# Kernel optimization log

Hardware: AMD Instinct MI355X
Metric: run time of the kernel (lower is better)

## Reference

```python
import jax, jax.numpy as jnp
import numpy as np

B, D, E = 65536, 1024, 16
H1, H2 = 128, 64          # expert hidden dims (hidden_dim=128, hidden_dim//2)
R1, R2 = 64, 32           # router hidden dims
EPS = 1e-5                # BatchNorm eps


def setup_inputs() -> dict:
    key = jax.random.key(0)
    ks = jax.random.split(key, 16)
    s = 0.02
    inp = {
        "x": jax.random.normal(ks[0], (B, D), jnp.float32),
        # router BatchNorm1d (eval mode: running stats)
        "r_gamma": jnp.ones((D,), jnp.float32),
        "r_beta": jnp.zeros((D,), jnp.float32),
        "r_mean": jnp.zeros((D,), jnp.float32),
        "r_var": jnp.ones((D,), jnp.float32),
        # router MLP D->64->32->16
        "rW1": jax.random.normal(ks[1], (D, R1), jnp.float32) * s,
        "rb1": jnp.full((R1,), 0.1, jnp.float32),
        "rW2": jax.random.normal(ks[2], (R1, R2), jnp.float32) * s,
        "rb2": jnp.full((R2,), 0.1, jnp.float32),
        "rW3": jax.random.normal(ks[3], (R2, E), jnp.float32) * s,
        "rb3": jnp.full((E,), 0.1, jnp.float32),
        # per-expert BatchNorm1d (eval mode)
        "e_gamma": jnp.ones((E, D), jnp.float32),
        "e_beta": jnp.zeros((E, D), jnp.float32),
        "e_mean": jnp.zeros((E, D), jnp.float32),
        "e_var": jnp.ones((E, D), jnp.float32),
        # per-expert MLP D->128->64->1, stacked along expert dim
        "eW1": jax.random.normal(ks[4], (E, D, H1), jnp.float32) * s,
        "eb1": jnp.full((E, H1), 0.1, jnp.float32),
        "eW2": jax.random.normal(ks[5], (E, H1, H2), jnp.float32) * s,
        "eb2": jnp.full((E, H2), 0.1, jnp.float32),
        "eW3": jax.random.normal(ks[6], (E, H2, 1), jnp.float32) * s,
        "eb3": jnp.full((E, 1), 0.1, jnp.float32),
    }
    return inp


def reference(x, r_gamma, r_beta, r_mean, r_var, rW1, rb1, rW2, rb2, rW3, rb3,
              e_gamma, e_beta, e_mean, e_var, eW1, eb1, eW2, eb2, eW3, eb3):
    # ---- router: BN (eval) -> Linear/ReLU -> Linear/ReLU -> Linear -> softmax
    xn = (x - r_mean) * (r_gamma / jnp.sqrt(r_var + EPS)) + r_beta   # [B,D]
    h = jax.nn.relu(xn @ rW1 + rb1)
    h = jax.nn.relu(h @ rW2 + rb2)
    routing_weights = jax.nn.softmax(h @ rW3 + rb3, axis=1)          # [B,E]

    # ---- experts: fold per-expert BN into first linear to avoid [E,B,D] copy
    scale = e_gamma / jnp.sqrt(e_var + EPS)                          # [E,D]
    shift = e_beta - e_mean * scale                                  # [E,D]
    W1_eff = eW1 * scale[:, :, None]                                 # [E,D,H1]
    b1_eff = eb1 + jnp.einsum('ed,edh->eh', shift, eW1)              # [E,H1]

    h1 = jax.nn.relu(jnp.einsum('bd,edh->ebh', x, W1_eff) + b1_eff[:, None, :])  # [E,B,H1]
    h2 = jax.nn.relu(jnp.einsum('ebh,ehk->ebk', h1, eW2) + eb2[:, None, :])      # [E,B,H2]
    logits = jnp.einsum('ebk,eko->ebo', h2, eW3) + eb3[:, None, :]               # [E,B,1]
    expert_outputs = jax.nn.sigmoid(logits[:, :, 0]).T               # [B,E]

    weighted_pred = jnp.sum(routing_weights * expert_outputs, axis=1)  # [B]
    return weighted_pred, routing_weights, expert_outputs
```

## Files before the change

kernel.cpp:

```cpp
#include <hip/hip_runtime.h>


typedef unsigned short u16;
typedef __attribute__((ext_vector_type(8))) short bf16x8;
typedef __attribute__((ext_vector_type(4))) float f32x4;
typedef __attribute__((ext_vector_type(8))) unsigned short u16x8;
typedef __attribute__((ext_vector_type(4))) unsigned short u16x4;

#define MFMA16(a, b, c) __builtin_amdgcn_mfma_f32_16x16x32_bf16(a, b, c, 0, 0, 0)

#define B_ROWS 65536
#define DIM 1024
#define NE 16
#define EPS 1e-5f

__device__ inline u16 f2bf(float f) {
    union { float f; unsigned u; } c; c.f = f;
    unsigned u = c.u;
    return (u16)((u + 0x7fffu + ((u >> 16) & 1u)) >> 16);
}

__device__ inline void gload16(const u16* g, u16* s) {
    __builtin_amdgcn_global_load_lds(
        (const __attribute__((address_space(1))) unsigned int*)g,
        (__attribute__((address_space(3))) unsigned int*)s,
        16, 0, 0);
}


__device__ void body_prep_x(int blk, int tid, const float* __restrict__ x,
                            u16* __restrict__ xs_g, u16* __restrict__ lds) {
    int p = tid & 15, rloc = tid >> 4;
    int r_g = blk * 16 + rloc;
    int r = r_g & 127;
    int lb = p & 7;
    int phys = lb ^ (r & 7);
    const float* xrow = x + (size_t)r_g * 1024;
#pragma unroll
    for (int i = 0; i < 8; ++i) {
        int kc = 2 * i + (p >> 3);
        int c = kc * 64 + lb * 8;
        float4 f0 = *(const float4*)(xrow + c);
        float4 f1 = *(const float4*)(xrow + c + 4);
        u16x8 u;
        u[0] = f2bf(f0.x); u[1] = f2bf(f0.y); u[2] = f2bf(f0.z); u[3] = f2bf(f0.w);
        u[4] = f2bf(f1.x); u[5] = f2bf(f1.y); u[6] = f2bf(f1.z); u[7] = f2bf(f1.w);
        *(u16x8*)&lds[(kc * 16 + rloc) * 64 + phys * 8] = u;
    }
    __syncthreads();
    int rb = blk >> 3, R0 = (blk & 7) * 16;
    int tl = tid & 127, th = tid >> 7;
#pragma unroll
    for (int jj = 0; jj < 8; ++jj) {
        int kc = 2 * jj + th;
        u16x8 v = *(const u16x8*)&lds[kc * 1024 + tl * 8];
        *(u16x8*)&xs_g[(((size_t)(rb * 16 + kc) * 128 + R0 + (tl >> 3)) << 6) + (tl & 7) * 8] = v;
    }
}

__device__ void body_prep_w1s(int t, const float* __restrict__ eW1, const float* __restrict__ eg,
                              const float* __restrict__ ev, u16* __restrict__ w1s) {
    int p = t & 7, r = (t >> 3) & 127, kc = (t >> 10) & 15, e = t >> 14;
    int lb = p ^ (r & 7);
    u16x8 u;
#pragma unroll
    for (int j = 0; j < 8; ++j) {
        int d = kc * 64 + lb * 8 + j;
        float sc = eg[e * 1024 + d] * rsqrtf(ev[e * 1024 + d] + EPS);
        u[j] = f2bf(eW1[((size_t)e * 1024 + d) * 128 + r] * sc);
    }
    *(u16x8*)&w1s[((size_t)((e * 16 + kc) * 128 + r) << 6) + p * 8] = u;
}

__device__ void body_prep_b1(int g, int lane, const float* __restrict__ eW1,
                             const float* __restrict__ eg, const float* __restrict__ eb,
                             const float* __restrict__ em, const float* __restrict__ ev,
                             const float* __restrict__ eb1, float* __restrict__ b1e) {
    int e = g >> 7, h = g & 127;
    float s = 0.f;
    for (int d = lane; d < 1024; d += 64) {
        float sc = eg[e * 1024 + d] * rsqrtf(ev[e * 1024 + d] + EPS);
        float sh = eb[e * 1024 + d] - em[e * 1024 + d] * sc;
        s += sh * eW1[((size_t)e * 1024 + d) * 128 + h];
    }
#pragma unroll
    for (int m = 1; m < 64; m <<= 1) s += __shfl_xor(s, m, 64);
    if (lane == 0) b1e[e * 128 + h] = eb1[e * 128 + h] + s;
}

__device__ void body_prep_rw1s(int t, const float* __restrict__ rW1, const float* __restrict__ rg,
                               const float* __restrict__ rv, u16* __restrict__ rw1s) {
    int p = t & 7, r = (t >> 3) & 63, kc = t >> 9;
    int lb = p ^ (r & 7);
    u16x8 u;
#pragma unroll
    for (int j = 0; j < 8; ++j) {
        int d = kc * 64 + lb * 8 + j;
        float sc = rg[d] * rsqrtf(rv[d] + EPS);
        u[j] = f2bf(rW1[d * 64 + r] * sc);
    }
    *(u16x8*)&rw1s[((kc * 64 + r) << 6) + p * 8] = u;
}

__device__ void body_prep_rb1(int j, int lane, const float* __restrict__ rW1,
                              const float* __restrict__ rg, const float* __restrict__ rbta,
                              const float* __restrict__ rm, const float* __restrict__ rv,
                              const float* __restrict__ rb1, float* __restrict__ rb1e) {
    float s = 0.f;
    for (int d = lane; d < 1024; d += 64) {
        float sc = rg[d] * rsqrtf(rv[d] + EPS);
        float sh = rbta[d] - rm[d] * sc;
        s += sh * rW1[d * 64 + j];
    }
#pragma unroll
    for (int m = 1; m < 64; m <<= 1) s += __shfl_xor(s, m, 64);
    if (lane == 0) rb1e[j] = rb1[j] + s;
}

__device__ void body_prep_w2s(int t, const float* __restrict__ eW2, u16* __restrict__ w2s) {
    int p = t & 15, j = (t >> 4) & 63, e = t >> 10;
    int lb = p ^ (j & 7);
    int h0 = lb * 8;
    u16x8 u;
#pragma unroll
    for (int jj = 0; jj < 8; ++jj)
        u[jj] = f2bf(eW2[((size_t)e * 128 + h0 + jj) * 64 + j]);
    *(u16x8*)&w2s[((e * 64 + j) << 7) + p * 8] = u;
}

__global__ __launch_bounds__(256) void prep_all(
    const float* __restrict__ x, u16* __restrict__ xs_g,
    const float* __restrict__ eW1, const float* __restrict__ eg,
    const float* __restrict__ eb, const float* __restrict__ em,
    const float* __restrict__ ev, const float* __restrict__ eb1,
    u16* __restrict__ w1s, float* __restrict__ b1e,
    const float* __restrict__ rW1, const float* __restrict__ rg,
    const float* __restrict__ rbta, const float* __restrict__ rm,
    const float* __restrict__ rv, const float* __restrict__ rb1,
    u16* __restrict__ rw1s, float* __restrict__ rb1e,
    const float* __restrict__ eW2, u16* __restrict__ w2s) {
    __shared__ __align__(16) u16 lds[16384];
    int bid = blockIdx.x, tid = threadIdx.x;
    if (bid < 4096) {
        body_prep_x(bid, tid, x, xs_g, lds);
    } else if (bid < 5120) {
        body_prep_w1s((bid - 4096) * 256 + tid, eW1, eg, ev, w1s);
    } else if (bid < 5632) {
        body_prep_b1((bid - 5120) * 4 + (tid >> 6), tid & 63, eW1, eg, eb, em, ev, eb1, b1e);
    } else if (bid < 5664) {
        body_prep_rw1s((bid - 5632) * 256 + tid, rW1, rg, rv, rw1s);
    } else if (bid < 5680) {
        body_prep_rb1((bid - 5664) * 4 + (tid >> 6), tid & 63, rW1, rg, rbta, rm, rv, rb1, rb1e);
    } else {
        body_prep_w2s((bid - 5680) * 256 + tid, eW2, w2s);
    }
}

__global__ __launch_bounds__(256) void fused_main(
    const u16* __restrict__ xs_g, const u16* __restrict__ w1s,
    const float* __restrict__ b1e, const u16* __restrict__ w2s,
    const float* __restrict__ eb2, const float* __restrict__ eW3,
    const float* __restrict__ eb3, float* __restrict__ out_eo,
    const u16* __restrict__ rw1s, const float* __restrict__ rb1e,
    const float* __restrict__ rW2, const float* __restrict__ rb2,
    const float* __restrict__ rW3, const float* __restrict__ rb3,
    float* __restrict__ out_rw) {
    __shared__ __align__(16) char smem[53248];

    int tid = threadIdx.x;
    int wave = tid >> 6, lane = tid & 63;
    int quad = lane >> 4, l15 = lane & 15;

    if (blockIdx.x >= 512) {
        u16* sA = (u16*)smem;
        u16* sW2 = (u16*)(smem + 32768);
        int bid = blockIdx.x - 512;
        int e = bid & 15, rb = bid >> 4;
        int wm = wave & 1, wn = wave >> 1;

        f32x4 acc[4][4] = {};
        const u16* xg_base = xs_g + (size_t)rb * 131072;
        const u16* wg_base = w1s + (size_t)e * 131072;

        for (int kc = 0; kc < 16; ++kc) {
            const u16* xg = xg_base + kc * 8192;
            const u16* wg = wg_base + kc * 8192;
            int so = wave * 2048;
#pragma unroll
            for (int i = 0; i < 4; ++i) {
                gload16(xg + so + i * 512 + lane * 8, &sA[so + i * 512]);
                gload16(wg + so + i * 512 + lane * 8, &sA[8192 + so + i * 512]);
            }
            __syncthreads();
#pragma unroll
            for (int ks = 0; ks < 2; ++ks) {
                bf16x8 af[4], bfr[4];
#pragma unroll
                for (int s = 0; s < 4; ++s) {
                    int h = wm * 64 + s * 16 + l15;
                    int phys = (ks * 4 + quad) ^ (h & 7);
                    af[s] = *(const bf16x8*)&sA[8192 + h * 64 + phys * 8];
                }
#pragma unroll
                for (int t = 0; t < 4; ++t) {
                    int m = wn * 64 + t * 16 + l15;
                    int phys = (ks * 4 + quad) ^ (m & 7);
                    bfr[t] = *(const bf16x8*)&sA[m * 64 + phys * 8];
                }
#pragma unroll
                for (int s = 0; s < 4; ++s)
#pragma unroll
                    for (int t = 0; t < 4; ++t)
                        acc[s][t] = MFMA16(af[s], bfr[t], acc[s][t]);
            }
            __syncthreads();
        }

        {
            const u16* wg2 = w2s + e * 8192;
            int so = wave * 2048;
#pragma unroll
            for (int i = 0; i < 4; ++i)
                gload16(wg2 + so + i * 512 + lane * 8, &sW2[so + i * 512]);
        }
#pragma unroll
        for (int s = 0; s < 4; ++s) {
            int h0 = wm * 64 + s * 16 + quad * 4;
            float4 bv = *(const float4*)&b1e[e * 128 + h0];
            float bva[4] = {bv.x, bv.y, bv.z, bv.w};
#pragma unroll
            for (int t = 0; t < 4; ++t) {
                int m = wn * 64 + t * 16 + l15;
                u16x4 pk;
#pragma unroll
                for (int r = 0; r < 4; ++r) {
                    float v = acc[s][t][r] + bva[r];
                    pk[r] = f2bf(fmaxf(v, 0.f));
                }
                int phys = (h0 >> 3) ^ (m & 7);
                *(u16x4*)&sA[m * 128 + phys * 8 + (h0 & 7)] = pk;
            }
        }
        __syncthreads();

        f32x4 acc2[2][4] = {};
#pragma unroll
        for (int ks = 0; ks < 4; ++ks) {
            bf16x8 a2[2], b2[4];
#pragma unroll
            for (int s = 0; s < 2; ++s) {
                int m = wave * 32 + s * 16 + l15;
                int phys = (ks * 4 + quad) ^ (m & 7);
                a2[s] = *(const bf16x8*)&sA[m * 128 + phys * 8];
            }
#pragma unroll
            for (int t = 0; t < 4; ++t) {
                int j = t * 16 + l15;
                int phys = (ks * 4 + quad) ^ (j & 7);
                b2[t] = *(const bf16x8*)&sW2[j * 128 + phys * 8];
            }
#pragma unroll
            for (int s = 0; s < 2; ++s)
#pragma unroll
                for (int t = 0; t < 4; ++t)
                    acc2[s][t] = MFMA16(a2[s], b2[t], acc2[s][t]);
        }

        float b2v[4], w3v[4];
#pragma unroll
        for (int t = 0; t < 4; ++t) {
            int j = t * 16 + l15;
            b2v[t] = eb2[e * 64 + j];
            w3v[t] = eW3[e * 64 + j];
        }
        float be3 = eb3[e];
#pragma unroll
        for (int s = 0; s < 2; ++s) {
            float sv[4] = {0.f, 0.f, 0.f, 0.f};
#pragma unroll
            for (int t = 0; t < 4; ++t)
#pragma unroll
                for (int r = 0; r < 4; ++r) {
                    float v = acc2[s][t][r] + b2v[t];
                    sv[r] += fmaxf(v, 0.f) * w3v[t];
                }
#pragma unroll
            for (int mask = 1; mask < 16; mask <<= 1)
#pragma unroll
                for (int r = 0; r < 4; ++r) sv[r] += __shfl_xor(sv[r], mask, 64);
            if (l15 == 0) {
#pragma unroll
                for (int r = 0; r < 4; ++r) {
                    int m = wave * 32 + s * 16 + quad * 4 + r;
                    float z = sv[r] + be3;
                    out_eo[(size_t)(rb * 128 + m) * 16 + e] = 1.f / (1.f + __expf(-z));
                }
            }
        }
    } else {
        char* region0 = smem;
        float* h2s = (float*)(smem + 34816);
        u16* xs_l = (u16*)region0;
        u16* rw_l = (u16*)(region0 + 16384);
        float* h_r = (float*)region0;
        int rb = blockIdx.x;

        f32x4 acc[4][2] = {};
        const u16* xg_base = xs_g + (size_t)rb * 131072;

        for (int kc = 0; kc < 16; ++kc) {
            const u16* xg = xg_base + kc * 8192;
            const u16* rg = rw1s + kc * 4096;
            int so = wave * 2048;
#pragma unroll
            for (int i = 0; i < 4; ++i)
                gload16(xg + so + i * 512 + lane * 8, &xs_l[so + i * 512]);
            int so2 = wave * 1024;
#pragma unroll
            for (int i = 0; i < 2; ++i)
                gload16(rg + so2 + i * 512 + lane * 8, &rw_l[so2 + i * 512]);
            __syncthreads();
#pragma unroll
            for (int ks = 0; ks < 2; ++ks) {
                bf16x8 af[4], bfr[2];
#pragma unroll
                for (int s = 0; s < 4; ++s) {
                    int j = s * 16 + l15;
                    int phys = (ks * 4 + quad) ^ (j & 7);
                    af[s] = *(const bf16x8*)&rw_l[j * 64 + phys * 8];
                }
#pragma unroll
                for (int t = 0; t < 2; ++t) {
                    int m = wave * 32 + t * 16 + l15;
                    int phys = (ks * 4 + quad) ^ (m & 7);
                    bfr[t] = *(const bf16x8*)&xs_l[m * 64 + phys * 8];
                }
#pragma unroll
                for (int s = 0; s < 4; ++s)
#pragma unroll
                    for (int t = 0; t < 2; ++t)
                        acc[s][t] = MFMA16(af[s], bfr[t], acc[s][t]);
            }
            __syncthreads();
        }

#pragma unroll
        for (int s = 0; s < 4; ++s) {
            int j0 = s * 16 + quad * 4;
            float4 bv = *(const float4*)&rb1e[j0];
#pragma unroll
            for (int t = 0; t < 2; ++t) {
                int m = wave * 32 + t * 16 + l15;
                float4 hv;
                hv.x = fmaxf(acc[s][t][0] + bv.x, 0.f);
                hv.y = fmaxf(acc[s][t][1] + bv.y, 0.f);
                hv.z = fmaxf(acc[s][t][2] + bv.z, 0.f);
                hv.w = fmaxf(acc[s][t][3] + bv.w, 0.f);
                *(float4*)&h_r[m * 68 + j0] = hv;
            }
        }
        __syncthreads();

        {
            int m = tid & 127, qg = tid >> 7;
            float h2r[16];
#pragma unroll
            for (int k = 0; k < 16; ++k) h2r[k] = 0.f;
            for (int i = 0; i < 64; ++i) {
                float hv = h_r[m * 68 + i];
                const float4* wrow = (const float4*)&rW2[i * 32 + qg * 16];
                float w[16];
                *(float4*)&w[0] = wrow[0];
                *(float4*)&w[4] = wrow[1];
                *(float4*)&w[8] = wrow[2];
                *(float4*)&w[12] = wrow[3];
#pragma unroll
                for (int k = 0; k < 16; ++k) h2r[k] += hv * w[k];
            }
#pragma unroll
            for (int k = 0; k < 16; ++k)
                h2r[k] = fmaxf(h2r[k] + rb2[qg * 16 + k], 0.f);
#pragma unroll
            for (int k = 0; k < 16; k += 4)
                *(float4*)&h2s[m * 36 + qg * 16 + k] = *(float4*)&h2r[k];
        }
        __syncthreads();

        if (tid < 128) {
            int mm = tid;
            float lg[16];
#pragma unroll
            for (int o = 0; o < 16; ++o) lg[o] = 0.f;
            for (int q = 0; q < 32; ++q) {
                float hv = h2s[mm * 36 + q];
                const float4* wr = (const float4*)&rW3[q * 16];
                float w[16];
                *(float4*)&w[0] = wr[0];
                *(float4*)&w[4] = wr[1];
                *(float4*)&w[8] = wr[2];
                *(float4*)&w[12] = wr[3];
#pragma unroll
                for (int o = 0; o < 16; ++o) lg[o] += hv * w[o];
            }
#pragma unroll
            for (int o = 0; o < 16; ++o) lg[o] += rb3[o];
            float mx = lg[0];
#pragma unroll
            for (int o = 1; o < 16; ++o) mx = fmaxf(mx, lg[o]);
            float ss = 0.f;
#pragma unroll
            for (int o = 0; o < 16; ++o) { lg[o] = __expf(lg[o] - mx); ss += lg[o]; }
            float inv = 1.f / ss;
            size_t base = (size_t)(rb * 128 + mm) * 16;
#pragma unroll
            for (int o = 0; o < 16; o += 4) {
                float4 v;
                v.x = lg[o] * inv; v.y = lg[o + 1] * inv;
                v.z = lg[o + 2] * inv; v.w = lg[o + 3] * inv;
                *(float4*)&out_rw[base + o] = v;
            }
        }
    }
}

__global__ void combine_kernel(const float* __restrict__ rw, const float* __restrict__ eo,
                               float* __restrict__ wp) {
    int b = blockIdx.x * 256 + threadIdx.x;
    const float4* r4 = (const float4*)(rw + (size_t)b * 16);
    const float4* o4 = (const float4*)(eo + (size_t)b * 16);
    float s = 0.f;
#pragma unroll
    for (int k = 0; k < 4; ++k) {
        float4 r = r4[k], o = o4[k];
        s += r.x * o.x + r.y * o.y + r.z * o.z + r.w * o.w;
    }
    wp[b] = s;
}


extern "C" void kernel_launch(void* const* d_in, const int* in_sizes, int n_in,
                              void* d_out, int out_size, void* d_ws, size_t ws_size,
                              hipStream_t stream) {
    const float* x       = (const float*)d_in[0];
    const float* r_gamma = (const float*)d_in[1];
    const float* r_beta  = (const float*)d_in[2];
    const float* r_mean  = (const float*)d_in[3];
    const float* r_var   = (const float*)d_in[4];
    const float* rW1     = (const float*)d_in[5];
    const float* rb1     = (const float*)d_in[6];
    const float* rW2     = (const float*)d_in[7];
    const float* rb2     = (const float*)d_in[8];
    const float* rW3     = (const float*)d_in[9];
    const float* rb3     = (const float*)d_in[10];
    const float* e_gamma = (const float*)d_in[11];
    const float* e_beta  = (const float*)d_in[12];
    const float* e_mean  = (const float*)d_in[13];
    const float* e_var   = (const float*)d_in[14];
    const float* eW1     = (const float*)d_in[15];
    const float* eb1     = (const float*)d_in[16];
    const float* eW2     = (const float*)d_in[17];
    const float* eb2     = (const float*)d_in[18];
    const float* eW3     = (const float*)d_in[19];
    const float* eb3     = (const float*)d_in[20];

    char* ws = (char*)d_ws;
    u16* xs_g   = (u16*)ws;
    u16* w1s    = (u16*)(ws + 134217728);
    u16* rw1s   = (u16*)(ws + 138412032);
    u16* w2s    = (u16*)(ws + 138543104);
    float* b1e  = (float*)(ws + 138805248);
    float* rb1e = (float*)(ws + 138813440);

    float* out_wp = (float*)d_out;
    float* out_rw = out_wp + B_ROWS;
    float* out_eo = out_rw + (size_t)B_ROWS * NE;

    prep_all<<<5744, 256, 0, stream>>>(
        x, xs_g,
        eW1, e_gamma, e_beta, e_mean, e_var, eb1, w1s, b1e,
        rW1, r_gamma, r_beta, r_mean, r_var, rb1, rw1s, rb1e,
        eW2, w2s);

    fused_main<<<8704, 256, 0, stream>>>(
        xs_g, w1s, b1e, w2s, eb2, eW3, eb3, out_eo,
        rw1s, rb1e, rW2, rb2, rW3, rb3, out_rw);

    combine_kernel<<<256, 256, 0, stream>>>(out_rw, out_eo, out_wp);
}
```

Baseline: 779.8 us.

## Reorder router blocks last, widen router tile to 256 rows, fuse router tail

Router blocks now come after the expert blocks in the grid, and each handles 256 rows instead of 128. This halves the router block count and reuses each loaded rW1 chunk across twice as many rows. The layer-1 hidden activations are stored in shared memory as bf16 to fit the smaller LDS footprint. Layers 2 and 3 now run per thread with no intermediate shared buffer or barrier. The costs are more registers per thread (32+16 accumulators), an extra bf16 rounding of the router hidden state, and router work scheduled at the tail of the grid, where it may create a tail imbalance.

```diff
diff --git a/kernel.cpp b/kernel.cpp
--- a/kernel.cpp
+++ b/kernel.cpp
@@ -18,6 +18,11 @@
     union { float f; unsigned u; } c; c.f = f;
     unsigned u = c.u;
     return (u16)((u + 0x7fffu + ((u >> 16) & 1u)) >> 16);
+}
+
+__device__ inline float bf2f(u16 v) {
+    union { unsigned u; float f; } c; c.u = ((unsigned)v) << 16;
+    return c.f;
 }
 
 __device__ inline void gload16(const u16* g, u16* s) {
@@ -165,16 +170,16 @@
     const float* __restrict__ rW2, const float* __restrict__ rb2,
     const float* __restrict__ rW3, const float* __restrict__ rb3,
     float* __restrict__ out_rw) {
-    __shared__ __align__(16) char smem[53248];
+    __shared__ __align__(16) char smem[49152];
 
     int tid = threadIdx.x;
     int wave = tid >> 6, lane = tid & 63;
     int quad = lane >> 4, l15 = lane & 15;
 
-    if (blockIdx.x >= 512) {
+    if (blockIdx.x < 8192) {
         u16* sA = (u16*)smem;
         u16* sW2 = (u16*)(smem + 32768);
-        int bid = blockIdx.x - 512;
+        int bid = blockIdx.x;
         int e = bid & 15, rb = bid >> 4;
         int wm = wave & 1, wn = wave >> 1;
 
@@ -298,31 +303,30 @@
             }
         }
     } else {
-        char* region0 = smem;
-        float* h2s = (float*)(smem + 34816);
-        u16* xs_l = (u16*)region0;
-        u16* rw_l = (u16*)(region0 + 16384);
-        float* h_r = (float*)region0;
-        int rb = blockIdx.x;
-
-        f32x4 acc[4][2] = {};
-        const u16* xg_base = xs_g + (size_t)rb * 131072;
+        int blk = blockIdx.x - 8192;
+        u16* xs_l = (u16*)smem;
+        u16* rw_l = (u16*)(smem + 32768);
+        u16* h_r = (u16*)smem;
+
+        f32x4 acc[4][4] = {};
+        const u16* xg0 = xs_g + (size_t)(2 * blk) * 131072;
+        const u16* xg1 = xg0 + 131072;
+        int chunk = wave >> 1;
 
         for (int kc = 0; kc < 16; ++kc) {
-            const u16* xg = xg_base + kc * 8192;
-            const u16* rg = rw1s + kc * 4096;
-            int so = wave * 2048;
-#pragma unroll
-            for (int i = 0; i < 4; ++i)
-                gload16(xg + so + i * 512 + lane * 8, &xs_l[so + i * 512]);
-            int so2 = wave * 1024;
+            const u16* src = (chunk == 0 ? xg0 : xg1) + kc * 8192 + (wave & 1) * 4096;
+            int dst = wave * 4096;
+#pragma unroll
+            for (int i = 0; i < 8; ++i)
+                gload16(src + i * 512 + lane * 8, &xs_l[dst + i * 512]);
+            const u16* rg = rw1s + kc * 4096 + wave * 1024;
 #pragma unroll
             for (int i = 0; i < 2; ++i)
-                gload16(rg + so2 + i * 512 + lane * 8, &rw_l[so2 + i * 512]);
+                gload16(rg + i * 512 + lane * 8, &rw_l[wave * 1024 + i * 512]);
             __syncthreads();
 #pragma unroll
             for (int ks = 0; ks < 2; ++ks) {
-                bf16x8 af[4], bfr[2];
+                bf16x8 af[4], bfr[4];
 #pragma unroll
                 for (int s = 0; s < 4; ++s) {
                     int j = s * 16 + l15;
@@ -330,15 +334,15 @@
                     af[s] = *(const bf16x8*)&rw_l[j * 64 + phys * 8];
                 }
 #pragma unroll
-                for (int t = 0; t < 2; ++t) {
-                    int m = wave * 32 + t * 16 + l15;
-                    int phys = (ks * 4 + quad) ^ (m & 7);
-                    bfr[t] = *(const bf16x8*)&xs_l[m * 64 + phys * 8];
+                for (int t = 0; t < 4; ++t) {
+                    int r = (wave & 1) * 64 + t * 16 + l15;
+                    int phys = (ks * 4 + quad) ^ (r & 7);
+                    bfr[t] = *(const bf16x8*)&xs_l[chunk * 8192 + r * 64 + phys * 8];
                 }
 #pragma unroll
                 for (int s = 0; s < 4; ++s)
 #pragma unroll
-                    for (int t = 0; t < 2; ++t)
+                    for (int t = 0; t < 4; ++t)
                         acc[s][t] = MFMA16(af[s], bfr[t], acc[s][t]);
             }
             __syncthreads();
@@ -348,59 +352,47 @@
         for (int s = 0; s < 4; ++s) {
             int j0 = s * 16 + quad * 4;
             float4 bv = *(const float4*)&rb1e[j0];
-#pragma unroll
-            for (int t = 0; t < 2; ++t) {
-                int m = wave * 32 + t * 16 + l15;
-                float4 hv;
-                hv.x = fmaxf(acc[s][t][0] + bv.x, 0.f);
-                hv.y = fmaxf(acc[s][t][1] + bv.y, 0.f);
-                hv.z = fmaxf(acc[s][t][2] + bv.z, 0.f);
-                hv.w = fmaxf(acc[s][t][3] + bv.w, 0.f);
-                *(float4*)&h_r[m * 68 + j0] = hv;
+            float bva[4] = {bv.x, bv.y, bv.z, bv.w};
+#pragma unroll
+            for (int t = 0; t < 4; ++t) {
+                int m = wave * 64 + t * 16 + l15;
+                u16x4 pk;
+#pragma unroll
+                for (int r = 0; r < 4; ++r)
+                    pk[r] = f2bf(fmaxf(acc[s][t][r] + bva[r], 0.f));
+                *(u16x4*)&h_r[m * 68 + j0] = pk;
             }
         }
         __syncthreads();
 
         {
-            int m = tid & 127, qg = tid >> 7;
-            float h2r[16];
-#pragma unroll
-            for (int k = 0; k < 16; ++k) h2r[k] = 0.f;
+            int m = tid;
+            float h2r[32];
+#pragma unroll
+            for (int k = 0; k < 32; ++k) h2r[k] = 0.f;
             for (int i = 0; i < 64; ++i) {
-                float hv = h_r[m * 68 + i];
-                const float4* wrow = (const float4*)&rW2[i * 32 + qg * 16];
-                float w[16];
-                *(float4*)&w[0] = wrow[0];
-                *(float4*)&w[4] = wrow[1];
-                *(float4*)&w[8] = wrow[2];
-                *(float4*)&w[12] = wrow[3];
-#pragma unroll
-                for (int k = 0; k < 16; ++k) h2r[k] += hv * w[k];
-            }
-#pragma unroll
-            for (int k = 0; k < 16; ++k)
-                h2r[k] = fmaxf(h2r[k] + rb2[qg * 16 + k], 0.f);
-#pragma unroll
-            for (int k = 0; k < 16; k += 4)
-                *(float4*)&h2s[m * 36 + qg * 16 + k] = *(float4*)&h2r[k];
-        }
-        __syncthreads();
-
-        if (tid < 128) {
-            int mm = tid;
+                float hv = bf2f(h_r[m * 68 + i]);
+                const float4* wrow = (const float4*)&rW2[i * 32];
+                float w[32];
+#pragma unroll
+                for (int q = 0; q < 8; ++q) *(float4*)&w[q * 4] = wrow[q];
+#pragma unroll
+                for (int k = 0; k < 32; ++k) h2r[k] += hv * w[k];
+            }
+#pragma unroll
+            for (int k = 0; k < 32; ++k)
+                h2r[k] = fmaxf(h2r[k] + rb2[k], 0.f);
+
             float lg[16];
 #pragma unroll
             for (int o = 0; o < 16; ++o) lg[o] = 0.f;
             for (int q = 0; q < 32; ++q) {
-                float hv = h2s[mm * 36 + q];
                 const float4* wr = (const float4*)&rW3[q * 16];
                 float w[16];
-                *(float4*)&w[0] = wr[0];
-                *(float4*)&w[4] = wr[1];
-                *(float4*)&w[8] = wr[2];
-                *(float4*)&w[12] = wr[3];
-#pragma unroll
-                for (int o = 0; o < 16; ++o) lg[o] += hv * w[o];
+#pragma unroll
+                for (int u = 0; u < 4; ++u) *(float4*)&w[u * 4] = wr[u];
+#pragma unroll
+                for (int o = 0; o < 16; ++o) lg[o] += h2r[q] * w[o];
             }
 #pragma unroll
             for (int o = 0; o < 16; ++o) lg[o] += rb3[o];
@@ -411,7 +403,7 @@
 #pragma unroll
             for (int o = 0; o < 16; ++o) { lg[o] = __expf(lg[o] - mx); ss += lg[o]; }
             float inv = 1.f / ss;
-            size_t base = (size_t)(rb * 128 + mm) * 16;
+            size_t base = (size_t)(blk * 256 + m) * 16;
 #pragma unroll
             for (int o = 0; o < 16; o += 4) {
                 float4 v;
@@ -481,7 +473,7 @@
         rW1, r_gamma, r_beta, r_mean, r_var, rb1, rw1s, rb1e,
         eW2, w2s);
 
-    fused_main<<<8704, 256, 0, stream>>>(
+    fused_main<<<8448, 256, 0, stream>>>(
         xs_g, w1s, b1e, w2s, eb2, eW3, eb3, out_eo,
         rw1s, rb1e, rW2, rb2, rW3, rb3, out_rw);
 
```

Result: no change. 790.5 us (+1.4%).
